# Performance work log

Measured on AMD Instinct MI355X. Metric: run time of the kernel, lower is better.

## Reference

```python
import jax, jax.numpy as jnp
import numpy as np

D_MODEL = 1024
N_HEADS = 16
D_K = D_MODEL // N_HEADS
EPS = 1e-8


def _l2_rownorm(x):
    # RowNormActivation: normalize each row (last dim) to unit L2 norm
    return x * jax.lax.rsqrt(jnp.sum(x * x, axis=-1, keepdims=True) + EPS)


def setup_inputs() -> dict:
    key = jax.random.key(0)
    ks = jax.random.split(key, 11)
    B, S = 2, 2048
    sc = 1.0 / np.sqrt(D_MODEL)
    inp = {
        "Q": jax.random.normal(ks[0], (B, S, D_MODEL), jnp.float32),
        "K": jax.random.normal(ks[1], (B, S, D_MODEL), jnp.float32),
        "V": jax.random.normal(ks[2], (B, S, D_MODEL), jnp.float32),
        "Wq_w": jax.random.normal(ks[3], (D_MODEL, D_MODEL), jnp.float32) * sc,
        "Wq_b": jnp.zeros((D_MODEL,), jnp.float32),
        "Wk_w": jax.random.normal(ks[4], (D_MODEL, D_MODEL), jnp.float32) * sc,
        "Wk_b": jnp.zeros((D_MODEL,), jnp.float32),
        "Wv_w": jax.random.normal(ks[5], (D_MODEL, D_MODEL), jnp.float32) * sc,
        "Wv_b": jnp.zeros((D_MODEL,), jnp.float32),
        "Wo_w": jax.random.normal(ks[6], (D_MODEL, D_MODEL), jnp.float32) * sc,
        "Wo_b": jnp.zeros((D_MODEL,), jnp.float32),
    }
    return inp


def reference(Q, K, V, Wq_w, Wq_b, Wk_w, Wk_b, Wv_w, Wv_b, Wo_w, Wo_b):
    B, S, _ = Q.shape
    # torch Linear: y = x @ W.T + b
    q = (Q @ Wq_w.T + Wq_b).reshape(B, S, N_HEADS, D_K).transpose(0, 2, 1, 3)
    k = (K @ Wk_w.T + Wk_b).reshape(B, S, N_HEADS, D_K).transpose(0, 2, 1, 3)
    v = (V @ Wv_w.T + Wv_b).reshape(B, S, N_HEADS, D_K).transpose(0, 2, 1, 3)
    qn = _l2_rownorm(q)
    kn = _l2_rownorm(k)
    scores = jnp.einsum("bhqd,bhkd->bhqk", qn, kn)
    attn = scores * scores  # squared similarity, no softmax (dropout=0 / eval)
    out = jnp.einsum("bhqk,bhkd->bhqd", attn, v)
    out = out.transpose(0, 2, 1, 3).reshape(B, S, D_MODEL)
    return out @ Wo_w.T + Wo_b
```

## Files before the change

### kernel.cpp

```cpp
#include <hip/hip_runtime.h>
#include <hip/hip_bf16.h>


#define D_MODEL 1024
#define N_HEADS 16
#define D_K     64
#define BATCH   2
#define SEQ     2048
#define M_TOT   (BATCH * SEQ)

typedef short  s16x8 __attribute__((ext_vector_type(8)));
typedef short  s16x4 __attribute__((ext_vector_type(4)));
typedef float  f32x4 __attribute__((ext_vector_type(4)));
typedef unsigned short ushort_t;
typedef ushort_t us4 __attribute__((ext_vector_type(4)));
typedef ushort_t us8 __attribute__((ext_vector_type(8)));

__device__ __forceinline__ ushort_t f2bf(float f) {
    union { float f; unsigned int u; } x; x.f = f;
    unsigned int u = x.u;
    return (ushort_t)((u + 0x7fffu + ((u >> 16) & 1u)) >> 16);
}
__device__ __forceinline__ float bf2f(ushort_t h) {
    union { unsigned int u; float f; } x; x.u = ((unsigned int)h) << 16;
    return x.f;
}
__device__ __forceinline__ unsigned int pack2bf(float a, float b) {
    union { __hip_bfloat162 h; unsigned int u; } x;
    x.h = __float22bfloat162_rn(float2{a, b});
    return x.u;
}

__device__ __forceinline__ f32x4 mfma_pv(s16x4 a, s16x4 b, f32x4 c) {
#if __has_builtin(__builtin_amdgcn_mfma_f32_16x16x16bf16_1k)
    return __builtin_amdgcn_mfma_f32_16x16x16bf16_1k(a, b, c, 0, 0, 0);
#else
    s16x8 a8 = {a[0], a[1], a[2], a[3], 0, 0, 0, 0};
    s16x8 b8 = {b[0], b[1], b[2], b[3], 0, 0, 0, 0};
    return __builtin_amdgcn_mfma_f32_16x16x32_bf16(a8, b8, c, 0, 0, 0);
#endif
}

__device__ __forceinline__ void gload_lds16(const ushort_t* g, ushort_t* l) {
    __builtin_amdgcn_global_load_lds(
        (__attribute__((address_space(1))) void*)(ushort_t*)g,
        (__attribute__((address_space(3))) void*)l, 16, 0, 0);
}

#define WAIT_VM(n)  asm volatile("s_waitcnt vmcnt(" #n ")" ::: "memory")
#define WAIT_LGKM0  asm volatile("s_waitcnt lgkmcnt(0)" ::: "memory")
#define BARRIER     asm volatile("s_barrier" ::: "memory")

struct ConvArgs {
    const float* src[11];
    ushort_t*    dst[11];
    int          n[11];
    int          cum[12];
};

__global__ __launch_bounds__(256) void convert_kernel(ConvArgs a) {
    const int lin = blockIdx.x;
    int t = 0;
#pragma unroll
    for (int i = 0; i < 11; ++i)
        if (lin >= a.cum[i + 1]) t = i + 1;
    const int off = (lin - a.cum[t]) * 2048 + threadIdx.x * 8;
    if (off >= a.n[t]) return;
    const float4 v0 = *(const float4*)(a.src[t] + off);
    const float4 v1 = *(const float4*)(a.src[t] + off + 4);
    us8 p;
    p[0] = f2bf(v0.x); p[1] = f2bf(v0.y); p[2] = f2bf(v0.z); p[3] = f2bf(v0.w);
    p[4] = f2bf(v1.x); p[5] = f2bf(v1.y); p[6] = f2bf(v1.z); p[7] = f2bf(v1.w);
    *(us8*)(a.dst[t] + off) = p;
}

template <int BM, int MODE>
__device__ __forceinline__ void gemm_body(
    ushort_t* __restrict__ smem,
    const ushort_t* __restrict__ A,
    const ushort_t* __restrict__ W,
    const ushort_t* __restrict__ bias,
    ushort_t* __restrict__ out,
    float* __restrict__ outf,
    int bx, int by)
{
    static_assert(BM == 64 || BM == 128, "");
    constexpr int K    = 1024;
    constexpr int MF   = BM / 32;
    constexpr int BUFW = (BM + 128) * 64;
    constexpr int NIT  = K / 64;

    const int t    = threadIdx.x;
    const int wave = t >> 6;
    const int lane = t & 63;
    const int quad = lane >> 4;
    const int lc   = lane & 15;
    const int wm   = wave >> 1;
    const int wn   = wave & 1;
    const int m0   = bx * BM;
    const int n0   = by * 128;

    f32x4 acc[MF][4];
    const f32x4 zero = {0.f, 0.f, 0.f, 0.f};
#pragma unroll
    for (int i = 0; i < MF; ++i)
#pragma unroll
        for (int j = 0; j < 4; ++j) acc[i][j] = zero;

    auto stage = [&](int buf, int k0) {
        ushort_t* Ast = smem + buf * BUFW;
        ushort_t* Bst = Ast + BM * 64;
#pragma unroll
        for (int c = 0; c < MF; ++c) {
            int idx = c * 256 + t;
            int row = idx >> 3, phys = idx & 7;
            int col = (phys ^ (row & 7)) * 8;
            gload_lds16(A + (size_t)(m0 + row) * K + k0 + col, Ast + idx * 8);
        }
#pragma unroll
        for (int c = 0; c < 4; ++c) {
            int idx = c * 256 + t;
            int row = idx >> 3, phys = idx & 7;
            int col = (phys ^ (row & 7)) * 8;
            gload_lds16(W + (size_t)(n0 + row) * K + k0 + col, Bst + idx * 8);
        }
    };
    auto loadfrags = [&](int buf, s16x8 (&a)[MF][2], s16x8 (&b)[4][2]) {
        ushort_t* Ast = smem + buf * BUFW;
        ushort_t* Bst = Ast + BM * 64;
#pragma unroll
        for (int ks = 0; ks < 2; ++ks) {
            const int ph = ((ks * 4 + quad) ^ (lc & 7)) * 8;
#pragma unroll
            for (int i = 0; i < MF; ++i)
                a[i][ks] = *(const s16x8*)(Ast + (wm * (BM / 2) + i * 16 + lc) * 64 + ph);
#pragma unroll
            for (int i = 0; i < 4; ++i)
                b[i][ks] = *(const s16x8*)(Bst + (wn * 64 + i * 16 + lc) * 64 + ph);
        }
    };
    auto mfmas = [&](s16x8 (&a)[MF][2], s16x8 (&b)[4][2]) {
#pragma unroll
        for (int ks = 0; ks < 2; ++ks)
#pragma unroll
            for (int mf = 0; mf < MF; ++mf)
#pragma unroll
                for (int nf = 0; nf < 4; ++nf)
                    acc[mf][nf] = __builtin_amdgcn_mfma_f32_16x16x32_bf16(
                        a[mf][ks], b[nf][ks], acc[mf][nf], 0, 0, 0);
    };

    stage(0, 0);
    stage(1, 64);
    s16x8 afr[MF][2], bfr[4][2];
    for (int it = 0; it < NIT; ++it) {
        if (it < NIT - 1) {
            if constexpr (BM == 128) WAIT_VM(8); else WAIT_VM(6);
        } else {
            WAIT_VM(0);
        }
        BARRIER;
        loadfrags(it & 1, afr, bfr);
        WAIT_LGKM0;
        BARRIER;
        if (it < NIT - 2) stage(it & 1, (it + 2) * 64);
        mfmas(afr, bfr);
    }

    float bv[4];
#pragma unroll
    for (int nf = 0; nf < 4; ++nf) bv[nf] = bf2f(bias[n0 + wn * 64 + nf * 16 + lc]);

    if (MODE == 0) {
#pragma unroll
        for (int mf = 0; mf < MF; ++mf)
#pragma unroll
            for (int nf = 0; nf < 4; ++nf)
#pragma unroll
                for (int r = 0; r < 4; ++r) {
                    int mg = m0 + wm * (BM / 2) + mf * 16 + quad * 4 + r;
                    int ng = n0 + wn * 64 + nf * 16 + lc;
                    outf[(size_t)mg * D_MODEL + ng] = acc[mf][nf][r] + bv[nf];
                }
    } else if (MODE == 1) {
#pragma unroll
        for (int mf = 0; mf < MF; ++mf)
#pragma unroll
            for (int r = 0; r < 4; ++r) {
                float ss = 0.f;
#pragma unroll
                for (int nf = 0; nf < 4; ++nf) {
                    float v = acc[mf][nf][r] + bv[nf];
                    acc[mf][nf][r] = v;
                    ss += v * v;
                }
                ss += __shfl_xor(ss, 1);
                ss += __shfl_xor(ss, 2);
                ss += __shfl_xor(ss, 4);
                ss += __shfl_xor(ss, 8);
                float inv = rsqrtf(ss + 1e-8f);
                int mg = m0 + wm * (BM / 2) + mf * 16 + quad * 4 + r;
                int b  = mg >> 11;
                int s  = mg & 2047;
#pragma unroll
                for (int nf = 0; nf < 4; ++nf) {
                    int ng = n0 + wn * 64 + nf * 16 + lc;
                    int h = ng >> 6, d = ng & 63;
                    out[(((size_t)(b * N_HEADS + h)) * SEQ + s) * D_K + d] =
                        f2bf(acc[mf][nf][r] * inv);
                }
            }
    } else {
        __syncthreads();
        ushort_t* vt = smem + wave * (64 * 72);
#pragma unroll
        for (int mf = 0; mf < 4; ++mf)
#pragma unroll
            for (int nf = 0; nf < 4; ++nf) {
                us4 p;
#pragma unroll
                for (int r = 0; r < 4; ++r) p[r] = f2bf(acc[mf][nf][r] + bv[nf]);
                *(us4*)(vt + (nf * 16 + lc) * 72 + mf * 16 + quad * 4) = p;
            }
        WAIT_LGKM0;
#pragma unroll
        for (int r = 0; r < 8; ++r) {
            int d  = r * 8 + (lane >> 3);
            int so = (lane & 7) * 8;
            uint4 val = *(const uint4*)(vt + d * 72 + so);
            int mg = m0 + wm * 64 + so;
            int b  = mg >> 11;
            int s  = mg & 2047;
            int ng = n0 + wn * 64 + d;
            int h = ng >> 6, dh = ng & 63;
            *(uint4*)(out + (((size_t)(b * N_HEADS + h)) * D_K + dh) * SEQ + s) = val;
        }
    }
}

__global__ __launch_bounds__(256) void qkv_kernel(
    const ushort_t* __restrict__ Qb, const ushort_t* __restrict__ Kb,
    const ushort_t* __restrict__ Vb,
    const ushort_t* __restrict__ Wq, const ushort_t* __restrict__ Wk,
    const ushort_t* __restrict__ Wv,
    const ushort_t* __restrict__ bq, const ushort_t* __restrict__ bk,
    const ushort_t* __restrict__ bv,
    ushort_t* __restrict__ qn, ushort_t* __restrict__ kn,
    ushort_t* __restrict__ vT)
{
    __shared__ __align__(16) ushort_t smem[2 * (128 + 128) * 64];
    const int lin = blockIdx.x;
    const int by  = lin & 7;
    const int r   = lin >> 3;
    const int bx  = r & 31;
    const int z   = r >> 5;
    if (z == 0)
        gemm_body<128, 1>(smem, Qb, Wq, bq, qn, nullptr, bx, by);
    else if (z == 1)
        gemm_body<128, 1>(smem, Kb, Wk, bk, kn, nullptr, bx, by);
    else
        gemm_body<128, 2>(smem, Vb, Wv, bv, vT, nullptr, bx, by);
}

__global__ __launch_bounds__(256) void wo_kernel(
    const ushort_t* __restrict__ A, const ushort_t* __restrict__ W,
    const ushort_t* __restrict__ bias, float* __restrict__ outf)
{
    __shared__ __align__(16) ushort_t smem[2 * (64 + 128) * 64];
    const int lin = blockIdx.x;
    gemm_body<64, 0>(smem, A, W, bias, nullptr, outf, lin >> 3, lin & 7);
}

__global__ __launch_bounds__(256, 2) void attn_kernel(
    const ushort_t* __restrict__ qn,
    const ushort_t* __restrict__ kn,
    const ushort_t* __restrict__ vT,
    ushort_t* __restrict__ attn_out)
{
    __shared__ __align__(16) ushort_t smem[4 * 8192];

    const int t    = threadIdx.x;
    const int wave = t >> 6;
    const int lane = t & 63;
    const int quad = lane >> 4;
    const int lc   = lane & 15;
    const int bh   = blockIdx.x;
    const int qt   = blockIdx.y;
    const int b    = bh >> 4;
    const int h    = bh & 15;

    const ushort_t* qb = qn + (size_t)bh * SEQ * D_K;
    const ushort_t* kb = kn + (size_t)bh * SEQ * D_K;
    const ushort_t* vb = vT + (size_t)bh * D_K * SEQ;
    const int q0 = qt * 128;

    s16x8 qf[8][2];
#pragma unroll
    for (int mf = 0; mf < 8; ++mf)
#pragma unroll
        for (int ks = 0; ks < 2; ++ks)
            qf[mf][ks] = *(const s16x8*)(qb + (size_t)(q0 + mf * 16 + lc) * D_K +
                                         ks * 32 + quad * 8);

    f32x4 oacc[4][8];
    const f32x4 zero = {0.f, 0.f, 0.f, 0.f};
#pragma unroll
    for (int df = 0; df < 4; ++df)
#pragma unroll
        for (int mf = 0; mf < 8; ++mf) oacc[df][mf] = zero;

    auto stage = [&](int buf, int j0) {
        ushort_t* kst = smem + buf * 8192;
        ushort_t* vst = kst + 4096;
#pragma unroll
        for (int c = 0; c < 2; ++c) {
            int idx = c * 256 + t;
            int row = idx >> 3, phys = idx & 7;
            int col = (phys ^ (row & 7)) * 8;
            gload_lds16(kb + (size_t)(j0 + row) * D_K + col, kst + idx * 8);
            gload_lds16(vb + (size_t)row * SEQ + j0 + col, vst + idx * 8);
        }
    };

    auto compute = [&](int buf) {
        ushort_t* kst = smem + buf * 8192;
        ushort_t* vst = kst + 4096;
        s16x8 ak[2];
#pragma unroll
        for (int ks = 0; ks < 2; ++ks)
            ak[ks] = *(const s16x8*)(kst + (wave * 16 + lc) * 64 +
                                     (((ks * 4 + quad) ^ (lc & 7)) * 8));
        s16x4 av[4];
#pragma unroll
        for (int df = 0; df < 4; ++df) {
            const int d  = df * 16 + lc;
            const int cj = wave * 2 + (quad >> 1);
            av[df] = *(const s16x4*)(vst + d * 64 + ((cj ^ (d & 7)) << 3) +
                                     ((quad & 1) << 2));
        }
#pragma unroll
        for (int mf = 0; mf < 8; ++mf) {
            f32x4 st = zero;
#pragma unroll
            for (int ks = 0; ks < 2; ++ks)
                st = __builtin_amdgcn_mfma_f32_16x16x32_bf16(ak[ks], qf[mf][ks],
                                                             st, 0, 0, 0);
            union { unsigned int u[2]; s16x4 v; } pb;
            pb.u[0] = pack2bf(st[0] * st[0], st[1] * st[1]);
            pb.u[1] = pack2bf(st[2] * st[2], st[3] * st[3]);
#pragma unroll
            for (int df = 0; df < 4; ++df)
                oacc[df][mf] = mfma_pv(av[df], pb.v, oacc[df][mf]);
        }
    };

    constexpr int NT = 32;
    stage(0, 0);
    stage(1, 64);
    stage(2, 128);
    for (int it = 0; it < NT; ++it) {
        if (it < NT - 2)      { WAIT_VM(8); }
        else if (it == NT - 2){ WAIT_VM(4); }
        else                  { WAIT_VM(0); }
        BARRIER;
        compute(it & 3);
        if (it < NT - 3) stage((it + 3) & 3, (it + 3) * 64);
    }

    float* red = (float*)smem;
    constexpr int RP = 17;
#pragma unroll
    for (int mf = 0; mf < 8; ++mf) {
        BARRIER;
#pragma unroll
        for (int df = 0; df < 4; ++df)
#pragma unroll
            for (int r = 0; r < 4; ++r)
                red[(wave * 64 + df * 16 + quad * 4 + r) * RP + lc] =
                    oacc[df][mf][r];
        WAIT_LGKM0;
        BARRIER;
#pragma unroll
        for (int qq = 0; qq < 4; ++qq) {
            const int q = wave * 4 + qq;
            const int d = lane;
            float v = red[(0 * 64 + d) * RP + q] + red[(1 * 64 + d) * RP + q] +
                      red[(2 * 64 + d) * RP + q] + red[(3 * 64 + d) * RP + q];
            const int s = q0 + mf * 16 + q;
            attn_out[((size_t)(b * SEQ + s)) * D_MODEL + h * D_K + d] = f2bf(v);
        }
    }
}

extern "C" void kernel_launch(void* const* d_in, const int* in_sizes, int n_in,
                              void* d_out, int out_size, void* d_ws, size_t ws_size,
                              hipStream_t stream)
{
    const float* Qf   = (const float*)d_in[0];
    const float* Kf   = (const float*)d_in[1];
    const float* Vf   = (const float*)d_in[2];
    const float* Wqf  = (const float*)d_in[3];
    const float* Wqbf = (const float*)d_in[4];
    const float* Wkf  = (const float*)d_in[5];
    const float* Wkbf = (const float*)d_in[6];
    const float* Wvf  = (const float*)d_in[7];
    const float* Wvbf = (const float*)d_in[8];
    const float* Wof  = (const float*)d_in[9];
    const float* Wobf = (const float*)d_in[10];

    const size_t NM = (size_t)M_TOT * D_MODEL;
    const size_t NW = (size_t)D_MODEL * D_MODEL;
    const size_t NB = D_MODEL;

    ushort_t* p = (ushort_t*)d_ws;
    ushort_t* Qb  = p;  p += NM;
    ushort_t* Kb  = p;  p += NM;
    ushort_t* Vb  = p;  p += NM;
    ushort_t* Wq  = p;  p += NW;
    ushort_t* Wk  = p;  p += NW;
    ushort_t* Wv  = p;  p += NW;
    ushort_t* Wo  = p;  p += NW;
    ushort_t* bq  = p;  p += NB;
    ushort_t* bk  = p;  p += NB;
    ushort_t* bvv = p;  p += NB;
    ushort_t* bo  = p;  p += NB;
    ushort_t* qn  = p;  p += NM;
    ushort_t* kn  = p;  p += NM;
    ushort_t* vT  = p;  p += NM;
    ushort_t* ao  = p;  p += NM;

    ConvArgs ca;
    ca.src[0] = Qf;   ca.dst[0] = Qb;  ca.n[0] = (int)NM;
    ca.src[1] = Kf;   ca.dst[1] = Kb;  ca.n[1] = (int)NM;
    ca.src[2] = Vf;   ca.dst[2] = Vb;  ca.n[2] = (int)NM;
    ca.src[3] = Wqf;  ca.dst[3] = Wq;  ca.n[3] = (int)NW;
    ca.src[4] = Wkf;  ca.dst[4] = Wk;  ca.n[4] = (int)NW;
    ca.src[5] = Wvf;  ca.dst[5] = Wv;  ca.n[5] = (int)NW;
    ca.src[6] = Wof;  ca.dst[6] = Wo;  ca.n[6] = (int)NW;
    ca.src[7] = Wqbf; ca.dst[7] = bq;  ca.n[7] = (int)NB;
    ca.src[8] = Wkbf; ca.dst[8] = bk;  ca.n[8] = (int)NB;
    ca.src[9] = Wvbf; ca.dst[9] = bvv; ca.n[9] = (int)NB;
    ca.src[10] = Wobf; ca.dst[10] = bo; ca.n[10] = (int)NB;

    int cum = 0;
    ca.cum[0] = 0;
    for (int i = 0; i < 11; ++i) {
        cum += (ca.n[i] + 2047) / 2048;
        ca.cum[i + 1] = cum;
    }

    dim3 blk(256);
    convert_kernel<<<dim3((unsigned)cum), blk, 0, stream>>>(ca);

    qkv_kernel<<<dim3(768), blk, 0, stream>>>(
        Qb, Kb, Vb, Wq, Wk, Wv, bq, bk, bvv, qn, kn, vT);
    attn_kernel<<<dim3(BATCH * N_HEADS, SEQ / 128), blk, 0, stream>>>(qn, kn, vT, ao);
    wo_kernel<<<dim3(512), blk, 0, stream>>>(
        ao, Wo, bo, (float*)d_out);
}
```

Baseline: 224.4 us.

## Fuse fp32-to-bf16 activation conversion into QKV GEMM A-tile loads

The QKV projection now reads fp32 Q/K/V directly, converts them to bf16 in registers and writes swizzled tiles to LDS. The separate conversion pass, with its extra round trip of three activation tensors through global memory, is dropped. The Wo GEMM tile also grows from 64 to 128 rows, halving its grid. The risks are a doubled A-tile read size from fp32 inside the GEMM, register-staged loads replacing async LDS loads, and a smaller Wo grid that may underfill the GPU.

```diff
diff --git a/kernel.cpp b/kernel.cpp
--- a/kernel.cpp
+++ b/kernel.cpp
@@ -52,17 +52,17 @@
 #define BARRIER     asm volatile("s_barrier" ::: "memory")
 
 struct ConvArgs {
-    const float* src[11];
-    ushort_t*    dst[11];
-    int          n[11];
-    int          cum[12];
+    const float* src[8];
+    ushort_t*    dst[8];
+    int          n[8];
+    int          cum[9];
 };
 
 __global__ __launch_bounds__(256) void convert_kernel(ConvArgs a) {
     const int lin = blockIdx.x;
     int t = 0;
 #pragma unroll
-    for (int i = 0; i < 11; ++i)
+    for (int i = 0; i < 8; ++i)
         if (lin >= a.cum[i + 1]) t = i + 1;
     const int off = (lin - a.cum[t]) * 2048 + threadIdx.x * 8;
     if (off >= a.n[t]) return;
@@ -182,7 +182,133 @@
                     int ng = n0 + wn * 64 + nf * 16 + lc;
                     outf[(size_t)mg * D_MODEL + ng] = acc[mf][nf][r] + bv[nf];
                 }
-    } else if (MODE == 1) {
+    }
+}
+
+template <int MODE>
+__device__ __forceinline__ void gemm_fused_body(
+    ushort_t* __restrict__ smem,
+    const float* __restrict__ Af,
+    const ushort_t* __restrict__ W,
+    const ushort_t* __restrict__ bias,
+    ushort_t* __restrict__ out,
+    int bx, int by)
+{
+    constexpr int BM   = 128;
+    constexpr int K    = 1024;
+    constexpr int MF   = 4;
+    constexpr int BUFW = (128 + 128) * 64;
+    constexpr int NIT  = 16;
+
+    const int t    = threadIdx.x;
+    const int wave = t >> 6;
+    const int lane = t & 63;
+    const int quad = lane >> 4;
+    const int lc   = lane & 15;
+    const int wm   = wave >> 1;
+    const int wn   = wave & 1;
+    const int m0   = bx * BM;
+    const int n0   = by * 128;
+
+    f32x4 acc[MF][4];
+    const f32x4 zero = {0.f, 0.f, 0.f, 0.f};
+#pragma unroll
+    for (int i = 0; i < MF; ++i)
+#pragma unroll
+        for (int j = 0; j < 4; ++j) acc[i][j] = zero;
+
+    float4 ar[8];
+    auto loadA = [&](int k0) {
+#pragma unroll
+        for (int c = 0; c < 4; ++c) {
+            int idx = c * 256 + t;
+            int row = idx >> 3, phys = idx & 7;
+            int col = (phys ^ (row & 7)) * 8;
+            const float* src = Af + (size_t)(m0 + row) * K + k0 + col;
+            ar[c * 2]     = *(const float4*)(src);
+            ar[c * 2 + 1] = *(const float4*)(src + 4);
+        }
+    };
+    auto writeA = [&](int buf) {
+        ushort_t* Ast = smem + buf * BUFW;
+#pragma unroll
+        for (int c = 0; c < 4; ++c) {
+            int idx = c * 256 + t;
+            us8 p;
+            p[0] = f2bf(ar[c * 2].x);     p[1] = f2bf(ar[c * 2].y);
+            p[2] = f2bf(ar[c * 2].z);     p[3] = f2bf(ar[c * 2].w);
+            p[4] = f2bf(ar[c * 2 + 1].x); p[5] = f2bf(ar[c * 2 + 1].y);
+            p[6] = f2bf(ar[c * 2 + 1].z); p[7] = f2bf(ar[c * 2 + 1].w);
+            *(us8*)(Ast + idx * 8) = p;
+        }
+    };
+    auto stageW = [&](int buf, int k0) {
+        ushort_t* Bst = smem + buf * BUFW + BM * 64;
+#pragma unroll
+        for (int c = 0; c < 4; ++c) {
+            int idx = c * 256 + t;
+            int row = idx >> 3, phys = idx & 7;
+            int col = (phys ^ (row & 7)) * 8;
+            gload_lds16(W + (size_t)(n0 + row) * K + k0 + col, Bst + idx * 8);
+        }
+    };
+    auto loadfrags = [&](int buf, s16x8 (&a)[MF][2], s16x8 (&b)[4][2]) {
+        ushort_t* Ast = smem + buf * BUFW;
+        ushort_t* Bst = Ast + BM * 64;
+#pragma unroll
+        for (int ks = 0; ks < 2; ++ks) {
+            const int ph = ((ks * 4 + quad) ^ (lc & 7)) * 8;
+#pragma unroll
+            for (int i = 0; i < MF; ++i)
+                a[i][ks] = *(const s16x8*)(Ast + (wm * 64 + i * 16 + lc) * 64 + ph);
+#pragma unroll
+            for (int i = 0; i < 4; ++i)
+                b[i][ks] = *(const s16x8*)(Bst + (wn * 64 + i * 16 + lc) * 64 + ph);
+        }
+    };
+    auto mfmas = [&](s16x8 (&a)[MF][2], s16x8 (&b)[4][2]) {
+#pragma unroll
+        for (int ks = 0; ks < 2; ++ks)
+#pragma unroll
+            for (int mf = 0; mf < MF; ++mf)
+#pragma unroll
+                for (int nf = 0; nf < 4; ++nf)
+                    acc[mf][nf] = __builtin_amdgcn_mfma_f32_16x16x32_bf16(
+                        a[mf][ks], b[nf][ks], acc[mf][nf], 0, 0, 0);
+    };
+
+    loadA(0);
+    stageW(0, 0);
+    WAIT_VM(4);
+    writeA(0);
+    loadA(64);
+    stageW(1, 64);
+    WAIT_VM(12);
+    WAIT_LGKM0;
+    BARRIER;
+
+    s16x8 afr[MF][2], bfr[4][2];
+    for (int it = 0; it < NIT; ++it) {
+        loadfrags(it & 1, afr, bfr);
+        if (it < NIT - 1) {
+            WAIT_VM(4);
+            writeA((it + 1) & 1);
+            WAIT_VM(0);
+        }
+        WAIT_LGKM0;
+        BARRIER;
+        if (it < NIT - 2) {
+            loadA((it + 2) * 64);
+            stageW(it & 1, (it + 2) * 64);
+        }
+        mfmas(afr, bfr);
+    }
+
+    float bv[4];
+#pragma unroll
+    for (int nf = 0; nf < 4; ++nf) bv[nf] = bf2f(bias[n0 + wn * 64 + nf * 16 + lc]);
+
+    if (MODE == 1) {
 #pragma unroll
         for (int mf = 0; mf < MF; ++mf)
 #pragma unroll
@@ -199,7 +325,7 @@
                 ss += __shfl_xor(ss, 4);
                 ss += __shfl_xor(ss, 8);
                 float inv = rsqrtf(ss + 1e-8f);
-                int mg = m0 + wm * (BM / 2) + mf * 16 + quad * 4 + r;
+                int mg = m0 + wm * 64 + mf * 16 + quad * 4 + r;
                 int b  = mg >> 11;
                 int s  = mg & 2047;
 #pragma unroll
@@ -223,6 +349,7 @@
                 *(us4*)(vt + (nf * 16 + lc) * 72 + mf * 16 + quad * 4) = p;
             }
         WAIT_LGKM0;
+        __syncthreads();
 #pragma unroll
         for (int r = 0; r < 8; ++r) {
             int d  = r * 8 + (lane >> 3);
@@ -239,8 +366,8 @@
 }
 
 __global__ __launch_bounds__(256) void qkv_kernel(
-    const ushort_t* __restrict__ Qb, const ushort_t* __restrict__ Kb,
-    const ushort_t* __restrict__ Vb,
+    const float* __restrict__ Qf, const float* __restrict__ Kf,
+    const float* __restrict__ Vf,
     const ushort_t* __restrict__ Wq, const ushort_t* __restrict__ Wk,
     const ushort_t* __restrict__ Wv,
     const ushort_t* __restrict__ bq, const ushort_t* __restrict__ bk,
@@ -255,20 +382,20 @@
     const int bx  = r & 31;
     const int z   = r >> 5;
     if (z == 0)
-        gemm_body<128, 1>(smem, Qb, Wq, bq, qn, nullptr, bx, by);
+        gemm_fused_body<1>(smem, Qf, Wq, bq, qn, bx, by);
     else if (z == 1)
-        gemm_body<128, 1>(smem, Kb, Wk, bk, kn, nullptr, bx, by);
+        gemm_fused_body<1>(smem, Kf, Wk, bk, kn, bx, by);
     else
-        gemm_body<128, 2>(smem, Vb, Wv, bv, vT, nullptr, bx, by);
+        gemm_fused_body<2>(smem, Vf, Wv, bv, vT, bx, by);
 }
 
 __global__ __launch_bounds__(256) void wo_kernel(
     const ushort_t* __restrict__ A, const ushort_t* __restrict__ W,
     const ushort_t* __restrict__ bias, float* __restrict__ outf)
 {
-    __shared__ __align__(16) ushort_t smem[2 * (64 + 128) * 64];
+    __shared__ __align__(16) ushort_t smem[2 * (128 + 128) * 64];
     const int lin = blockIdx.x;
-    gemm_body<64, 0>(smem, A, W, bias, nullptr, outf, lin >> 3, lin & 7);
+    gemm_body<128, 0>(smem, A, W, bias, nullptr, outf, lin >> 3, lin & 7);
 }
 
 __global__ __launch_bounds__(256, 2) void attn_kernel(
@@ -413,9 +540,6 @@
     const size_t NB = D_MODEL;
 
     ushort_t* p = (ushort_t*)d_ws;
-    ushort_t* Qb  = p;  p += NM;
-    ushort_t* Kb  = p;  p += NM;
-    ushort_t* Vb  = p;  p += NM;
     ushort_t* Wq  = p;  p += NW;
     ushort_t* Wk  = p;  p += NW;
     ushort_t* Wv  = p;  p += NW;
@@ -430,21 +554,18 @@
     ushort_t* ao  = p;  p += NM;
 
     ConvArgs ca;
-    ca.src[0] = Qf;   ca.dst[0] = Qb;  ca.n[0] = (int)NM;
-    ca.src[1] = Kf;   ca.dst[1] = Kb;  ca.n[1] = (int)NM;
-    ca.src[2] = Vf;   ca.dst[2] = Vb;  ca.n[2] = (int)NM;
-    ca.src[3] = Wqf;  ca.dst[3] = Wq;  ca.n[3] = (int)NW;
-    ca.src[4] = Wkf;  ca.dst[4] = Wk;  ca.n[4] = (int)NW;
-    ca.src[5] = Wvf;  ca.dst[5] = Wv;  ca.n[5] = (int)NW;
-    ca.src[6] = Wof;  ca.dst[6] = Wo;  ca.n[6] = (int)NW;
-    ca.src[7] = Wqbf; ca.dst[7] = bq;  ca.n[7] = (int)NB;
-    ca.src[8] = Wkbf; ca.dst[8] = bk;  ca.n[8] = (int)NB;
-    ca.src[9] = Wvbf; ca.dst[9] = bvv; ca.n[9] = (int)NB;
-    ca.src[10] = Wobf; ca.dst[10] = bo; ca.n[10] = (int)NB;
+    ca.src[0] = Wqf;  ca.dst[0] = Wq;  ca.n[0] = (int)NW;
+    ca.src[1] = Wkf;  ca.dst[1] = Wk;  ca.n[1] = (int)NW;
+    ca.src[2] = Wvf;  ca.dst[2] = Wv;  ca.n[2] = (int)NW;
+    ca.src[3] = Wof;  ca.dst[3] = Wo;  ca.n[3] = (int)NW;
+    ca.src[4] = Wqbf; ca.dst[4] = bq;  ca.n[4] = (int)NB;
+    ca.src[5] = Wkbf; ca.dst[5] = bk;  ca.n[5] = (int)NB;
+    ca.src[6] = Wvbf; ca.dst[6] = bvv; ca.n[6] = (int)NB;
+    ca.src[7] = Wobf; ca.dst[7] = bo;  ca.n[7] = (int)NB;
 
     int cum = 0;
     ca.cum[0] = 0;
-    for (int i = 0; i < 11; ++i) {
+    for (int i = 0; i < 8; ++i) {
         cum += (ca.n[i] + 2047) / 2048;
         ca.cum[i + 1] = cum;
     }
@@ -453,8 +574,8 @@
     convert_kernel<<<dim3((unsigned)cum), blk, 0, stream>>>(ca);
 
     qkv_kernel<<<dim3(768), blk, 0, stream>>>(
-        Qb, Kb, Vb, Wq, Wk, Wv, bq, bk, bvv, qn, kn, vT);
+        Qf, Kf, Vf, Wq, Wk, Wv, bq, bk, bvv, qn, kn, vT);
     attn_kernel<<<dim3(BATCH * N_HEADS, SEQ / 128), blk, 0, stream>>>(qn, kn, vT, ao);
-    wo_kernel<<<dim3(512), blk, 0, stream>>>(
+    wo_kernel<<<dim3(256), blk, 0, stream>>>(
         ao, Wo, bo, (float*)d_out);
 }
```

After: 257.7 us. 1.15x slower.
